# Optimization experiments

Measured on AMD Instinct MI355X. Metric: run time of the kernel, lower is better.

Reference implementation:

```python
import jax, jax.numpy as jnp
import numpy as np

B, S, D_IN, D_OUT, N_EXPERTS = 8, 4096, 512, 512, 8


def setup_inputs() -> dict:
    key = jax.random.key(0)
    k1, k2, k3, k4 = jax.random.split(key, 4)
    x = jax.random.normal(k1, (B, S, D_IN), dtype=jnp.float32)
    partitions = jax.random.randint(k2, (B, S), 0, N_EXPERTS, dtype=jnp.int32)
    # per-branch nn.Linear weights: [n, out_features, in_features], kaiming-ish scale
    W = jax.random.normal(k3, (N_EXPERTS, D_OUT, D_IN), dtype=jnp.float32) * 0.03
    b = jax.random.normal(k4, (N_EXPERTS, D_OUT), dtype=jnp.float32) * 0.01
    return {"x": x, "partitions": partitions, "W": W, "b": b}


def reference(x, partitions, W, b):
    # Hard token partition -> per-branch linear -> scatter combine.
    # Equivalent math to dynamic_partition + branch Linear + dynamic_stitch:
    # out[t] = x[t] @ W[p[t]].T + b[p[t]]
    in_shape = x.shape
    xf = x.reshape(-1, in_shape[-1])          # [T, d_in]
    p = partitions.reshape(-1)                # [T]
    # Compute all-expert outputs, then select per-token expert (vectorized
    # replacement for the variable-size per-partition GEMM loop).
    y = jnp.einsum('td,eod->teo', xf, W) + b[None, :, :]   # [T, n, d_out]
    out = jnp.take_along_axis(y, p[:, None, None], axis=1)[:, 0, :]  # [T, d_out]
    return out.reshape(in_shape[:-1] + (W.shape[1],))
```

## Files before the change

### kernel.cpp

```cpp
#include <hip/hip_runtime.h>
#include <hip/hip_bf16.h>

#define N_EXPERTS 8
#define T_TOKENS 32768
#define D 512
#define TILE 128
#define BK 64
#define NT 4
#define LT_MAX 256
#define GEMM_GRID (N_EXPERTS * LT_MAX * NT)
#define SCATTER_BLOCKS (T_TOKENS / 256)
#define CONVW_BLOCKS ((N_EXPERTS * D * D) / (8 * 256))

typedef __bf16 bf16x8 __attribute__((ext_vector_type(8)));
typedef float  f32x4  __attribute__((ext_vector_type(4)));
typedef unsigned short u16x8 __attribute__((ext_vector_type(8)));

__device__ __forceinline__ unsigned short f2bf(float f) {
    unsigned int u = __float_as_uint(f);
    u += 0x7FFFu + ((u >> 16) & 1u);
    return (unsigned short)(u >> 16);
}

__device__ __forceinline__ u16x8 cvt8(float4 a, float4 b) {
    u16x8 o;
    o[0] = f2bf(a.x); o[1] = f2bf(a.y); o[2] = f2bf(a.z); o[3] = f2bf(a.w);
    o[4] = f2bf(b.x); o[5] = f2bf(b.y); o[6] = f2bf(b.z); o[7] = f2bf(b.w);
    return o;
}

__device__ __forceinline__ void gl2lds16(const void* g, void* l) {
    __builtin_amdgcn_global_load_lds(
        (const __attribute__((address_space(1))) void*)g,
        (__attribute__((address_space(3))) void*)l, 16, 0, 0);
}

__global__ __launch_bounds__(256) void prep_kernel(
        const int* __restrict__ p, int* __restrict__ fill, int* __restrict__ sorted,
        const float* __restrict__ W, unsigned short* __restrict__ Wb) {
    int bid = blockIdx.x;
    int tid = threadIdx.x;
    if (bid < SCATTER_BLOCKS) {
        __shared__ int lcount[N_EXPERTS];
        __shared__ int lbase[N_EXPERTS];
        if (tid < N_EXPERTS) lcount[tid] = 0;
        __syncthreads();
        int t = bid * 256 + tid;
        int e = p[t];
        int lrank = atomicAdd(&lcount[e], 1);
        __syncthreads();
        if (tid < N_EXPERTS)
            lbase[tid] = (lcount[tid] > 0) ? atomicAdd(&fill[tid], lcount[tid]) : 0;
        __syncthreads();
        sorted[e * T_TOKENS + (lbase[e] + 1 + lrank)] = t;
    } else {
        size_t i = ((size_t)(bid - SCATTER_BLOCKS) * 256 + tid) * 8;
        float4 a = *(const float4*)(W + i);
        float4 b = *(const float4*)(W + i + 4);
        *(u16x8*)&Wb[i] = cvt8(a, b);
    }
}

__global__ __launch_bounds__(256, 3) void moe_gemm_fused(
        const float* __restrict__ x, const unsigned short* __restrict__ Wb,
        const float* __restrict__ bias, const int* __restrict__ fill,
        const int* __restrict__ sorted, float* __restrict__ out) {
    __shared__ int s_idx[TILE];
    __shared__ unsigned short sA[TILE * BK];
    __shared__ unsigned short sB[2][TILE * BK];

    int bid = blockIdx.x;
    int e = bid & 7;
    int cnt = fill[e] + 1;
    int j = bid >> 3;
    int lt = j >> 2, bn = j & 3;
    int row0 = lt * TILE;
    if (row0 >= cnt) return;

    int tid = threadIdx.x;
    if (tid < TILE) {
        int r = row0 + tid;
        s_idx[tid] = (r < cnt) ? sorted[e * T_TOKENS + r] : -1;
    }
    __syncthreads();

    int wave = tid >> 6, lane = tid & 63;
    int wm = (wave >> 1) * 64, wn = (wave & 1) * 64;
    int lrow = lane & 15, lq = lane >> 4;
    int srow = lane >> 3, scol = lane & 7, swz = scol ^ srow;

    const float* aptr[4];
#pragma unroll
    for (int t = 0; t < 4; t++) {
        int tok = s_idx[wave * 32 + t * 8 + srow];
        aptr[t] = x + (size_t)(tok < 0 ? 0 : tok) * D + swz * 8;
    }
    const unsigned short* gB = Wb + (size_t)e * D * D
                             + (size_t)(bn * TILE + wave * 32 + srow) * D + swz * 8;

#pragma unroll
    for (int t = 0; t < 4; t++)
        gl2lds16(gB + (size_t)(t * 8) * D, &sB[0][(wave * 32 + t * 8) * BK]);
    __builtin_amdgcn_sched_barrier(0);
    float4 pa[8];
#pragma unroll
    for (int t = 0; t < 4; t++) {
        pa[2 * t]     = *(const float4*)(aptr[t]);
        pa[2 * t + 1] = *(const float4*)(aptr[t] + 4);
    }

    f32x4 acc[4][4];
#pragma unroll
    for (int i = 0; i < 4; i++)
#pragma unroll
        for (int j2 = 0; j2 < 4; j2++)
            acc[i][j2] = (f32x4){0.f, 0.f, 0.f, 0.f};

#pragma unroll
    for (int step = 0; step < 8; step++) {
        const int kk = step * BK;
        asm volatile("s_waitcnt lgkmcnt(0)" ::: "memory");
        __builtin_amdgcn_s_barrier();
        __builtin_amdgcn_sched_barrier(0);
#pragma unroll
        for (int t = 0; t < 4; t++) {
            u16x8 av = cvt8(pa[2 * t], pa[2 * t + 1]);
            *(u16x8*)&sA[(wave * 32 + t * 8 + srow) * BK + scol * 8] = av;
        }
        __builtin_amdgcn_sched_barrier(0);
        if (step < 7) {
#pragma unroll
            for (int t = 0; t < 4; t++)
                gl2lds16(gB + (size_t)(t * 8) * D + kk + BK,
                         &sB[(step + 1) & 1][(wave * 32 + t * 8) * BK]);
            __builtin_amdgcn_sched_barrier(0);
#pragma unroll
            for (int t = 0; t < 4; t++) {
                pa[2 * t]     = *(const float4*)(aptr[t] + kk + BK);
                pa[2 * t + 1] = *(const float4*)(aptr[t] + kk + BK + 4);
            }
            __builtin_amdgcn_sched_barrier(0);
        }
        asm volatile("s_waitcnt lgkmcnt(0)" ::: "memory");
        __builtin_amdgcn_s_barrier();
        __builtin_amdgcn_sched_barrier(0);
        const unsigned short* sBc = sB[step & 1];
#pragma unroll
        for (int ks = 0; ks < 2; ks++) {
            bf16x8 af[4], bfr[4];
#pragma unroll
            for (int i = 0; i < 4; i++) {
                int row = wm + 16 * i + lrow;
                int cb = (ks * 4 + lq) ^ (lrow & 7);
                af[i] = *(const bf16x8*)&sA[row * BK + cb * 8];
            }
#pragma unroll
            for (int j2 = 0; j2 < 4; j2++) {
                int row = wn + 16 * j2 + lrow;
                int cb = (ks * 4 + lq) ^ (lrow & 7);
                bfr[j2] = *(const bf16x8*)&sBc[row * BK + cb * 8];
            }
#pragma unroll
            for (int i = 0; i < 4; i++)
#pragma unroll
                for (int j2 = 0; j2 < 4; j2++)
                    acc[i][j2] = __builtin_amdgcn_mfma_f32_16x16x32_bf16(
                        af[i], bfr[j2], acc[i][j2], 0, 0, 0);
        }
    }

#pragma unroll
    for (int j2 = 0; j2 < 4; j2++) {
        int ng = bn * TILE + wn + 16 * j2 + lrow;
        float bv = bias[e * D + ng];
#pragma unroll
        for (int i = 0; i < 4; i++) {
#pragma unroll
            for (int r = 0; r < 4; r++) {
                int mrow = wm + 16 * i + lq * 4 + r;
                int tok = s_idx[mrow];
                if (tok >= 0)
                    out[(size_t)tok * D + ng] = acc[i][j2][r] + bv;
            }
        }
    }
}

__global__ __launch_bounds__(256) void moe_gemm_f32(
        const float* __restrict__ x, const float* __restrict__ W,
        const float* __restrict__ bias, const int* __restrict__ fill,
        const int* __restrict__ sorted, float* __restrict__ out) {
    __shared__ int s_idx[TILE];
    __shared__ unsigned short sA[TILE][BK + 8];
    __shared__ unsigned short sB[TILE][BK + 8];

    int bid = blockIdx.x;
    int e = bid & 7;
    int cnt = fill[e] + 1;
    int j = bid >> 3;
    int lt = j >> 2, bn = j & 3;
    int row0 = lt * TILE;
    if (row0 >= cnt) return;

    int tid = threadIdx.x;
    if (tid < TILE) {
        int r = row0 + tid;
        s_idx[tid] = (r < cnt) ? sorted[e * T_TOKENS + r] : -1;
    }
    __syncthreads();

    const float* Wb = W + (size_t)e * D * D + (size_t)(bn * TILE) * D;

    f32x4 acc[4][4];
#pragma unroll
    for (int i = 0; i < 4; i++)
#pragma unroll
        for (int j2 = 0; j2 < 4; j2++)
            acc[i][j2] = (f32x4){0.f, 0.f, 0.f, 0.f};

    int wave = tid >> 6, lane = tid & 63;
    int wm = (wave >> 1) * 64, wn = (wave & 1) * 64;
    int lrow = lane & 15, lq = lane >> 4;

    for (int kk = 0; kk < D; kk += BK) {
#pragma unroll
        for (int i = 0; i < 8; i++) {
            int flat = tid + i * 256;
            int r = flat >> 4, c = (flat & 15) << 2;
            int tok = s_idx[r];
            float4 v = make_float4(0.f, 0.f, 0.f, 0.f);
            if (tok >= 0) v = *(const float4*)(x + (size_t)tok * D + kk + c);
            ushort4 w4;
            w4.x = f2bf(v.x); w4.y = f2bf(v.y); w4.z = f2bf(v.z); w4.w = f2bf(v.w);
            *(ushort4*)&sA[r][c] = w4;
        }
#pragma unroll
        for (int i = 0; i < 8; i++) {
            int flat = tid + i * 256;
            int r = flat >> 4, c = (flat & 15) << 2;
            float4 v = *(const float4*)(Wb + (size_t)r * D + kk + c);
            ushort4 w4;
            w4.x = f2bf(v.x); w4.y = f2bf(v.y); w4.z = f2bf(v.z); w4.w = f2bf(v.w);
            *(ushort4*)&sB[r][c] = w4;
        }
        __syncthreads();
#pragma unroll
        for (int ks = 0; ks < 2; ks++) {
            bf16x8 af[4], bfr[4];
#pragma unroll
            for (int i = 0; i < 4; i++)
                af[i] = *(const bf16x8*)&sA[wm + 16 * i + lrow][ks * 32 + lq * 8];
#pragma unroll
            for (int j2 = 0; j2 < 4; j2++)
                bfr[j2] = *(const bf16x8*)&sB[wn + 16 * j2 + lrow][ks * 32 + lq * 8];
#pragma unroll
            for (int i = 0; i < 4; i++)
#pragma unroll
                for (int j2 = 0; j2 < 4; j2++)
                    acc[i][j2] = __builtin_amdgcn_mfma_f32_16x16x32_bf16(
                        af[i], bfr[j2], acc[i][j2], 0, 0, 0);
        }
        __syncthreads();
    }

#pragma unroll
    for (int j2 = 0; j2 < 4; j2++) {
        int ng = bn * TILE + wn + 16 * j2 + lrow;
        float bv = bias[e * D + ng];
#pragma unroll
        for (int i = 0; i < 4; i++) {
#pragma unroll
            for (int r = 0; r < 4; r++) {
                int mrow = wm + 16 * i + lq * 4 + r;
                int tok = s_idx[mrow];
                if (tok >= 0)
                    out[(size_t)tok * D + ng] = acc[i][j2][r] + bv;
            }
        }
    }
}

extern "C" void kernel_launch(void* const* d_in, const int* in_sizes, int n_in,
                              void* d_out, int out_size, void* d_ws, size_t ws_size,
                              hipStream_t stream) {
    const float* x    = (const float*)d_in[0];
    const int*   part = (const int*)d_in[1];
    const float* W    = (const float*)d_in[2];
    const float* b    = (const float*)d_in[3];
    float* out = (float*)d_out;

    const size_t wb_elems     = (size_t)N_EXPERTS * D * D;
    const size_t sorted_elems = (size_t)N_EXPERTS * T_TOKENS;
    const size_t fast_bytes   = wb_elems * 2 + (sorted_elems + 8) * 4;
    const size_t slow_bytes   = (sorted_elems + 8) * 4;

    if (ws_size >= fast_bytes) {
        unsigned short* Wb = (unsigned short*)d_ws;
        int* sorted = (int*)(Wb + wb_elems);
        int* fill   = sorted + sorted_elems;

        hipMemsetAsync(fill, 0xFF, N_EXPERTS * sizeof(int), stream);
        prep_kernel<<<SCATTER_BLOCKS + CONVW_BLOCKS, 256, 0, stream>>>(
            part, fill, sorted, W, Wb);
        moe_gemm_fused<<<GEMM_GRID, 256, 0, stream>>>(x, Wb, b, fill, sorted, out);
    } else if (ws_size >= slow_bytes) {
        int* sorted = (int*)d_ws;
        int* fill   = sorted + sorted_elems;

        hipMemsetAsync(fill, 0xFF, N_EXPERTS * sizeof(int), stream);
        prep_kernel<<<SCATTER_BLOCKS, 256, 0, stream>>>(
            part, fill, sorted, W, (unsigned short*)nullptr);
        moe_gemm_f32<<<GEMM_GRID, 256, 0, stream>>>(x, W, b, fill, sorted, out);
    }
}
```

Measured before the change: 167.9 us.

## Pre-convert activations to bf16 and stream both GEMM operands via direct-to-LDS loads

The prep kernel now also converts x to a bf16 workspace copy. The GEMM kernel then loads both the gathered token rows and the weights with global_load_lds into a double-buffered LDS tile, removing per-step register conversion and the LDS writes for A. It also adds a wave priority bump around the MFMA block and lowers launch bounds to 2 waves per SIMD. The epilogue stages results through LDS so output rows are written as coalesced 16-byte stores. The cost is an extra full pass over x (read f32, write bf16), more workspace, and more LDS per block.

```diff
diff --git a/kernel.cpp b/kernel.cpp
--- a/kernel.cpp
+++ b/kernel.cpp
@@ -11,6 +11,7 @@
 #define GEMM_GRID (N_EXPERTS * LT_MAX * NT)
 #define SCATTER_BLOCKS (T_TOKENS / 256)
 #define CONVW_BLOCKS ((N_EXPERTS * D * D) / (8 * 256))
+#define CONVX_BLOCKS ((T_TOKENS * D) / (8 * 256))
 
 typedef __bf16 bf16x8 __attribute__((ext_vector_type(8)));
 typedef float  f32x4  __attribute__((ext_vector_type(4)));
@@ -37,7 +38,8 @@
 
 __global__ __launch_bounds__(256) void prep_kernel(
         const int* __restrict__ p, int* __restrict__ fill, int* __restrict__ sorted,
-        const float* __restrict__ W, unsigned short* __restrict__ Wb) {
+        const float* __restrict__ W, unsigned short* __restrict__ Wb,
+        const float* __restrict__ x, unsigned short* __restrict__ xb) {
     int bid = blockIdx.x;
     int tid = threadIdx.x;
     if (bid < SCATTER_BLOCKS) {
@@ -53,21 +55,25 @@
             lbase[tid] = (lcount[tid] > 0) ? atomicAdd(&fill[tid], lcount[tid]) : 0;
         __syncthreads();
         sorted[e * T_TOKENS + (lbase[e] + 1 + lrank)] = t;
-    } else {
+    } else if (bid < SCATTER_BLOCKS + CONVW_BLOCKS) {
         size_t i = ((size_t)(bid - SCATTER_BLOCKS) * 256 + tid) * 8;
         float4 a = *(const float4*)(W + i);
         float4 b = *(const float4*)(W + i + 4);
         *(u16x8*)&Wb[i] = cvt8(a, b);
-    }
-}
-
-__global__ __launch_bounds__(256, 3) void moe_gemm_fused(
-        const float* __restrict__ x, const unsigned short* __restrict__ Wb,
+    } else {
+        size_t i = ((size_t)(bid - SCATTER_BLOCKS - CONVW_BLOCKS) * 256 + tid) * 8;
+        float4 a = *(const float4*)(x + i);
+        float4 b = *(const float4*)(x + i + 4);
+        *(u16x8*)&xb[i] = cvt8(a, b);
+    }
+}
+
+__global__ __launch_bounds__(256, 2) void moe_gemm_dma(
+        const unsigned short* __restrict__ xb, const unsigned short* __restrict__ Wb,
         const float* __restrict__ bias, const int* __restrict__ fill,
         const int* __restrict__ sorted, float* __restrict__ out) {
     __shared__ int s_idx[TILE];
-    __shared__ unsigned short sA[TILE * BK];
-    __shared__ unsigned short sB[2][TILE * BK];
+    __shared__ unsigned short buf[2][2][TILE * BK];
 
     int bid = blockIdx.x;
     int e = bid & 7;
@@ -89,25 +95,22 @@
     int lrow = lane & 15, lq = lane >> 4;
     int srow = lane >> 3, scol = lane & 7, swz = scol ^ srow;
 
-    const float* aptr[4];
+    const unsigned short* gA[4];
 #pragma unroll
     for (int t = 0; t < 4; t++) {
         int tok = s_idx[wave * 32 + t * 8 + srow];
-        aptr[t] = x + (size_t)(tok < 0 ? 0 : tok) * D + swz * 8;
+        gA[t] = xb + (size_t)(tok < 0 ? 0 : tok) * D + swz * 8;
     }
     const unsigned short* gB = Wb + (size_t)e * D * D
                              + (size_t)(bn * TILE + wave * 32 + srow) * D + swz * 8;
 
-#pragma unroll
-    for (int t = 0; t < 4; t++)
-        gl2lds16(gB + (size_t)(t * 8) * D, &sB[0][(wave * 32 + t * 8) * BK]);
-    __builtin_amdgcn_sched_barrier(0);
-    float4 pa[8];
-#pragma unroll
-    for (int t = 0; t < 4; t++) {
-        pa[2 * t]     = *(const float4*)(aptr[t]);
-        pa[2 * t + 1] = *(const float4*)(aptr[t] + 4);
-    }
+#define STAGE(K, KB) do {                                                     \
+    _Pragma("unroll") for (int t = 0; t < 4; t++)                             \
+        gl2lds16(gA[t] + (K) * BK, &buf[KB][0][(wave * 32 + t * 8) * BK]);    \
+    _Pragma("unroll") for (int t = 0; t < 4; t++)                             \
+        gl2lds16(gB + (size_t)(t * 8) * D + (K) * BK,                         \
+                 &buf[KB][1][(wave * 32 + t * 8) * BK]);                      \
+} while (0)
 
     f32x4 acc[4][4];
 #pragma unroll
@@ -116,35 +119,25 @@
         for (int j2 = 0; j2 < 4; j2++)
             acc[i][j2] = (f32x4){0.f, 0.f, 0.f, 0.f};
 
+    STAGE(0, 0);
+
 #pragma unroll
     for (int step = 0; step < 8; step++) {
-        const int kk = step * BK;
         asm volatile("s_waitcnt lgkmcnt(0)" ::: "memory");
         __builtin_amdgcn_s_barrier();
         __builtin_amdgcn_sched_barrier(0);
-#pragma unroll
-        for (int t = 0; t < 4; t++) {
-            u16x8 av = cvt8(pa[2 * t], pa[2 * t + 1]);
-            *(u16x8*)&sA[(wave * 32 + t * 8 + srow) * BK + scol * 8] = av;
-        }
-        __builtin_amdgcn_sched_barrier(0);
         if (step < 7) {
-#pragma unroll
-            for (int t = 0; t < 4; t++)
-                gl2lds16(gB + (size_t)(t * 8) * D + kk + BK,
-                         &sB[(step + 1) & 1][(wave * 32 + t * 8) * BK]);
+            STAGE(step + 1, (step + 1) & 1);
             __builtin_amdgcn_sched_barrier(0);
-#pragma unroll
-            for (int t = 0; t < 4; t++) {
-                pa[2 * t]     = *(const float4*)(aptr[t] + kk + BK);
-                pa[2 * t + 1] = *(const float4*)(aptr[t] + kk + BK + 4);
-            }
-            __builtin_amdgcn_sched_barrier(0);
-        }
-        asm volatile("s_waitcnt lgkmcnt(0)" ::: "memory");
+            asm volatile("s_waitcnt vmcnt(8)" ::: "memory");
+        } else {
+            asm volatile("s_waitcnt vmcnt(0)" ::: "memory");
+        }
         __builtin_amdgcn_s_barrier();
         __builtin_amdgcn_sched_barrier(0);
-        const unsigned short* sBc = sB[step & 1];
+        const unsigned short* sA = buf[step & 1][0];
+        const unsigned short* sB = buf[step & 1][1];
+        __builtin_amdgcn_s_setprio(1);
 #pragma unroll
         for (int ks = 0; ks < 2; ks++) {
             bf16x8 af[4], bfr[4];
@@ -158,7 +151,7 @@
             for (int j2 = 0; j2 < 4; j2++) {
                 int row = wn + 16 * j2 + lrow;
                 int cb = (ks * 4 + lq) ^ (lrow & 7);
-                bfr[j2] = *(const bf16x8*)&sBc[row * BK + cb * 8];
+                bfr[j2] = *(const bf16x8*)&sB[row * BK + cb * 8];
             }
 #pragma unroll
             for (int i = 0; i < 4; i++)
@@ -167,21 +160,45 @@
                     acc[i][j2] = __builtin_amdgcn_mfma_f32_16x16x32_bf16(
                         af[i], bfr[j2], acc[i][j2], 0, 0, 0);
         }
-    }
+        __builtin_amdgcn_s_setprio(0);
+    }
+#undef STAGE
 
 #pragma unroll
     for (int j2 = 0; j2 < 4; j2++) {
-        int ng = bn * TILE + wn + 16 * j2 + lrow;
-        float bv = bias[e * D + ng];
-#pragma unroll
-        for (int i = 0; i < 4; i++) {
-#pragma unroll
-            for (int r = 0; r < 4; r++) {
-                int mrow = wm + 16 * i + lq * 4 + r;
-                int tok = s_idx[mrow];
-                if (tok >= 0)
-                    out[(size_t)tok * D + ng] = acc[i][j2][r] + bv;
-            }
+        float bv = bias[e * D + bn * TILE + wn + 16 * j2 + lrow];
+#pragma unroll
+        for (int i = 0; i < 4; i++)
+#pragma unroll
+            for (int r = 0; r < 4; r++)
+                acc[i][j2][r] += bv;
+    }
+
+    float* ct = (float*)&buf[0][0][0];
+#pragma unroll
+    for (int p = 0; p < 2; p++) {
+        asm volatile("s_waitcnt lgkmcnt(0)" ::: "memory");
+        __builtin_amdgcn_s_barrier();
+        if ((wave >> 1) == p) {
+#pragma unroll
+            for (int j2 = 0; j2 < 4; j2++)
+#pragma unroll
+                for (int i = 0; i < 4; i++)
+#pragma unroll
+                    for (int r = 0; r < 4; r++)
+                        ct[(16 * i + lq * 4 + r) * TILE + wn + 16 * j2 + lrow]
+                            = acc[i][j2][r];
+        }
+        asm volatile("s_waitcnt lgkmcnt(0)" ::: "memory");
+        __builtin_amdgcn_s_barrier();
+#pragma unroll
+        for (int k = 0; k < 8; k++) {
+            int u = tid + 256 * k;
+            int row = u >> 5, ch = u & 31;
+            int tok = s_idx[p * 64 + row];
+            f32x4 v = *(const f32x4*)&ct[row * TILE + ch * 4];
+            if (tok >= 0)
+                *(f32x4*)&out[(size_t)tok * D + bn * TILE + ch * 4] = v;
         }
     }
 }
@@ -209,7 +226,7 @@
     }
     __syncthreads();
 
-    const float* Wb = W + (size_t)e * D * D + (size_t)(bn * TILE) * D;
+    const float* Wbp = W + (size_t)e * D * D + (size_t)(bn * TILE) * D;
 
     f32x4 acc[4][4];
 #pragma unroll
@@ -238,7 +255,7 @@
         for (int i = 0; i < 8; i++) {
             int flat = tid + i * 256;
             int r = flat >> 4, c = (flat & 15) << 2;
-            float4 v = *(const float4*)(Wb + (size_t)r * D + kk + c);
+            float4 v = *(const float4*)(Wbp + (size_t)r * D + kk + c);
             ushort4 w4;
             w4.x = f2bf(v.x); w4.y = f2bf(v.y); w4.z = f2bf(v.z); w4.w = f2bf(v.w);
             *(ushort4*)&sB[r][c] = w4;
@@ -289,27 +306,30 @@
     const float* b    = (const float*)d_in[3];
     float* out = (float*)d_out;
 
+    const size_t xb_elems     = (size_t)T_TOKENS * D;
     const size_t wb_elems     = (size_t)N_EXPERTS * D * D;
     const size_t sorted_elems = (size_t)N_EXPERTS * T_TOKENS;
-    const size_t fast_bytes   = wb_elems * 2 + (sorted_elems + 8) * 4;
+    const size_t fast_bytes   = (xb_elems + wb_elems) * 2 + (sorted_elems + 8) * 4;
     const size_t slow_bytes   = (sorted_elems + 8) * 4;
 
     if (ws_size >= fast_bytes) {
-        unsigned short* Wb = (unsigned short*)d_ws;
+        unsigned short* xb = (unsigned short*)d_ws;
+        unsigned short* Wb = xb + xb_elems;
         int* sorted = (int*)(Wb + wb_elems);
         int* fill   = sorted + sorted_elems;
 
         hipMemsetAsync(fill, 0xFF, N_EXPERTS * sizeof(int), stream);
-        prep_kernel<<<SCATTER_BLOCKS + CONVW_BLOCKS, 256, 0, stream>>>(
-            part, fill, sorted, W, Wb);
-        moe_gemm_fused<<<GEMM_GRID, 256, 0, stream>>>(x, Wb, b, fill, sorted, out);
+        prep_kernel<<<SCATTER_BLOCKS + CONVW_BLOCKS + CONVX_BLOCKS, 256, 0, stream>>>(
+            part, fill, sorted, W, Wb, x, xb);
+        moe_gemm_dma<<<GEMM_GRID, 256, 0, stream>>>(xb, Wb, b, fill, sorted, out);
     } else if (ws_size >= slow_bytes) {
         int* sorted = (int*)d_ws;
         int* fill   = sorted + sorted_elems;
 
         hipMemsetAsync(fill, 0xFF, N_EXPERTS * sizeof(int), stream);
         prep_kernel<<<SCATTER_BLOCKS, 256, 0, stream>>>(
-            part, fill, sorted, W, (unsigned short*)nullptr);
+            part, fill, sorted, W, (unsigned short*)nullptr,
+            x, (unsigned short*)nullptr);
         moe_gemm_f32<<<GEMM_GRID, 256, 0, stream>>>(x, W, b, fill, sorted, out);
     }
 }
```

Result: faster. 153.6 us (-8.5%).

## Load A fragments directly to registers and compact the GEMM grid

Applied to the files above, without the earlier changes.

Replaces the fused GEMM with a variant where each wave loads its own A rows straight from global memory into MFMA register fragments, converting them to bf16 in registers and dropping the sA shared-memory round trip. The wave tiling changes from 64x64 to 32x128, so every wave reads all of B. The grid is compacted to a fixed count of workgroups that map onto the actual per-expert tiles, instead of launching the maximum grid and exiting early. Output goes through an LDS transpose so stores are coalesced 16-byte rows, and s_setprio is raised around the MFMA block. The cost is uncoalesced per-lane A loads and more LDS reads of B per wave.

```diff
diff --git a/kernel.cpp b/kernel.cpp
--- a/kernel.cpp
+++ b/kernel.cpp
@@ -9,6 +9,7 @@
 #define NT 4
 #define LT_MAX 256
 #define GEMM_GRID (N_EXPERTS * LT_MAX * NT)
+#define GRID_WG 1056
 #define SCATTER_BLOCKS (T_TOKENS / 256)
 #define CONVW_BLOCKS ((N_EXPERTS * D * D) / (8 * 256))
 
@@ -61,13 +62,172 @@
     }
 }
 
-__global__ __launch_bounds__(256, 3) void moe_gemm_fused(
+__global__ __launch_bounds__(256, 3) void moe_gemm_rs(
         const float* __restrict__ x, const unsigned short* __restrict__ Wb,
         const float* __restrict__ bias, const int* __restrict__ fill,
         const int* __restrict__ sorted, float* __restrict__ out) {
     __shared__ int s_idx[TILE];
-    __shared__ unsigned short sA[TILE * BK];
     __shared__ unsigned short sB[2][TILE * BK];
+
+    int bid = blockIdx.x;
+    int w6 = bid >> 3;
+    int m = (bid & 7) + (w6 >> 2) * 8;
+    int bn = w6 & 3;
+
+    int e = 0, lt = 0, tacc = 0, found = 0, cnt_e = 0;
+#pragma unroll
+    for (int i = 0; i < N_EXPERTS; i++) {
+        int c = fill[i] + 1;
+        int tiles = (c + TILE - 1) >> 7;
+        if (!found && m < tacc + tiles) { e = i; lt = m - tacc; cnt_e = c; found = 1; }
+        tacc += tiles;
+    }
+    if (!found) return;
+    int row0 = lt * TILE;
+
+    int tid = threadIdx.x;
+    if (tid < TILE) {
+        int r = row0 + tid;
+        s_idx[tid] = (r < cnt_e) ? sorted[e * T_TOKENS + r] : -1;
+    }
+    __syncthreads();
+
+    int wave = tid >> 6, lane = tid & 63;
+    int lrow = lane & 15, lq = lane >> 4;
+    int srow = lane >> 3, scol = lane & 7, swz = scol ^ srow;
+
+    const float* ax[2];
+#pragma unroll
+    for (int mb = 0; mb < 2; mb++) {
+        int tok = s_idx[wave * 32 + mb * 16 + lrow];
+        ax[mb] = x + (size_t)(tok < 0 ? 0 : tok) * D + lq * 8;
+    }
+    const unsigned short* gB = Wb + (size_t)e * D * D
+                             + (size_t)(bn * TILE + wave * 32 + srow) * D + swz * 8;
+
+#define STAGE_B(K, KB) do {                                                   \
+    _Pragma("unroll") for (int t = 0; t < 4; t++)                             \
+        gl2lds16(gB + (size_t)(t * 8) * D + (K) * BK,                         \
+                 &sB[KB][(wave * 32 + t * 8) * BK]);                          \
+} while (0)
+
+#define LOAD_A(K, SB) do {                                                    \
+    _Pragma("unroll") for (int mb = 0; mb < 2; mb++)                          \
+    _Pragma("unroll") for (int ks = 0; ks < 2; ks++) {                        \
+        raw[SB][mb][ks][0] = *(const float4*)(ax[mb] + (K) * BK + ks * 32);   \
+        raw[SB][mb][ks][1] = *(const float4*)(ax[mb] + (K) * BK + ks * 32 + 4);\
+    }                                                                         \
+} while (0)
+
+    float4 raw[2][2][2][2];
+    f32x4 acc[2][8];
+#pragma unroll
+    for (int mb = 0; mb < 2; mb++)
+#pragma unroll
+        for (int nj = 0; nj < 8; nj++)
+            acc[mb][nj] = (f32x4){0.f, 0.f, 0.f, 0.f};
+
+    STAGE_B(0, 0);
+    __builtin_amdgcn_sched_barrier(0);
+    LOAD_A(0, 0);
+    __builtin_amdgcn_sched_barrier(0);
+
+#pragma unroll
+    for (int step = 0; step < 8; step++) {
+        asm volatile("s_waitcnt lgkmcnt(0)" ::: "memory");
+        __builtin_amdgcn_s_barrier();
+        __builtin_amdgcn_sched_barrier(0);
+        if (step < 7) {
+            STAGE_B(step + 1, (step + 1) & 1);
+            __builtin_amdgcn_sched_barrier(0);
+            asm volatile("s_waitcnt vmcnt(4)" ::: "memory");
+        } else {
+            asm volatile("s_waitcnt vmcnt(0)" ::: "memory");
+        }
+        __builtin_amdgcn_sched_barrier(0);
+        bf16x8 af[2][2];
+#pragma unroll
+        for (int mb = 0; mb < 2; mb++)
+#pragma unroll
+            for (int ks = 0; ks < 2; ks++) {
+                u16x8 t = cvt8(raw[step & 1][mb][ks][0], raw[step & 1][mb][ks][1]);
+                af[mb][ks] = *(bf16x8*)&t;
+            }
+        if (step < 7) {
+            LOAD_A(step + 1, (step + 1) & 1);
+            __builtin_amdgcn_sched_barrier(0);
+        }
+        __builtin_amdgcn_s_barrier();
+        __builtin_amdgcn_sched_barrier(0);
+        const unsigned short* sBc = sB[step & 1];
+        __builtin_amdgcn_s_setprio(1);
+#pragma unroll
+        for (int ks = 0; ks < 2; ks++) {
+            bf16x8 bfr[8];
+#pragma unroll
+            for (int nj = 0; nj < 8; nj++) {
+                int row = 16 * nj + lrow;
+                int cb = (ks * 4 + lq) ^ (lrow & 7);
+                bfr[nj] = *(const bf16x8*)&sBc[row * BK + cb * 8];
+            }
+#pragma unroll
+            for (int mb = 0; mb < 2; mb++)
+#pragma unroll
+                for (int nj = 0; nj < 8; nj++)
+                    acc[mb][nj] = __builtin_amdgcn_mfma_f32_16x16x32_bf16(
+                        af[mb][ks], bfr[nj], acc[mb][nj], 0, 0, 0);
+        }
+        __builtin_amdgcn_s_setprio(0);
+    }
+#undef STAGE_B
+#undef LOAD_A
+
+#pragma unroll
+    for (int nj = 0; nj < 8; nj++) {
+        float bv = bias[e * D + bn * TILE + 16 * nj + lrow];
+#pragma unroll
+        for (int mb = 0; mb < 2; mb++)
+#pragma unroll
+            for (int r = 0; r < 4; r++)
+                acc[mb][nj][r] += bv;
+    }
+
+    float* ct = (float*)&sB[0][0];
+#pragma unroll
+    for (int p = 0; p < 2; p++) {
+        asm volatile("s_waitcnt lgkmcnt(0)" ::: "memory");
+        __builtin_amdgcn_s_barrier();
+        if ((wave >> 1) == p) {
+#pragma unroll
+            for (int mb = 0; mb < 2; mb++)
+#pragma unroll
+                for (int nj = 0; nj < 8; nj++)
+#pragma unroll
+                    for (int r = 0; r < 4; r++)
+                        ct[((wave & 1) * 32 + 16 * mb + lq * 4 + r) * TILE
+                           + 16 * nj + lrow] = acc[mb][nj][r];
+        }
+        asm volatile("s_waitcnt lgkmcnt(0)" ::: "memory");
+        __builtin_amdgcn_s_barrier();
+#pragma unroll
+        for (int k = 0; k < 8; k++) {
+            int u = tid + 256 * k;
+            int row = u >> 5, ch = u & 31;
+            int tok = s_idx[p * 64 + row];
+            f32x4 v = *(const f32x4*)&ct[row * TILE + ch * 4];
+            if (tok >= 0)
+                *(f32x4*)&out[(size_t)tok * D + bn * TILE + ch * 4] = v;
+        }
+    }
+}
+
+__global__ __launch_bounds__(256) void moe_gemm_f32(
+        const float* __restrict__ x, const float* __restrict__ W,
+        const float* __restrict__ bias, const int* __restrict__ fill,
+        const int* __restrict__ sorted, float* __restrict__ out) {
+    __shared__ int s_idx[TILE];
+    __shared__ unsigned short sA[TILE][BK + 8];
+    __shared__ unsigned short sB[TILE][BK + 8];
 
     int bid = blockIdx.x;
     int e = bid & 7;
@@ -84,132 +244,7 @@
     }
     __syncthreads();
 
-    int wave = tid >> 6, lane = tid & 63;
-    int wm = (wave >> 1) * 64, wn = (wave & 1) * 64;
-    int lrow = lane & 15, lq = lane >> 4;
-    int srow = lane >> 3, scol = lane & 7, swz = scol ^ srow;
-
-    const float* aptr[4];
-#pragma unroll
-    for (int t = 0; t < 4; t++) {
-        int tok = s_idx[wave * 32 + t * 8 + srow];
-        aptr[t] = x + (size_t)(tok < 0 ? 0 : tok) * D + swz * 8;
-    }
-    const unsigned short* gB = Wb + (size_t)e * D * D
-                             + (size_t)(bn * TILE + wave * 32 + srow) * D + swz * 8;
-
-#pragma unroll
-    for (int t = 0; t < 4; t++)
-        gl2lds16(gB + (size_t)(t * 8) * D, &sB[0][(wave * 32 + t * 8) * BK]);
-    __builtin_amdgcn_sched_barrier(0);
-    float4 pa[8];
-#pragma unroll
-    for (int t = 0; t < 4; t++) {
-        pa[2 * t]     = *(const float4*)(aptr[t]);
-        pa[2 * t + 1] = *(const float4*)(aptr[t] + 4);
-    }
-
-    f32x4 acc[4][4];
-#pragma unroll
-    for (int i = 0; i < 4; i++)
-#pragma unroll
-        for (int j2 = 0; j2 < 4; j2++)
-            acc[i][j2] = (f32x4){0.f, 0.f, 0.f, 0.f};
-
-#pragma unroll
-    for (int step = 0; step < 8; step++) {
-        const int kk = step * BK;
-        asm volatile("s_waitcnt lgkmcnt(0)" ::: "memory");
-        __builtin_amdgcn_s_barrier();
-        __builtin_amdgcn_sched_barrier(0);
-#pragma unroll
-        for (int t = 0; t < 4; t++) {
-            u16x8 av = cvt8(pa[2 * t], pa[2 * t + 1]);
-            *(u16x8*)&sA[(wave * 32 + t * 8 + srow) * BK + scol * 8] = av;
-        }
-        __builtin_amdgcn_sched_barrier(0);
-        if (step < 7) {
-#pragma unroll
-            for (int t = 0; t < 4; t++)
-                gl2lds16(gB + (size_t)(t * 8) * D + kk + BK,
-                         &sB[(step + 1) & 1][(wave * 32 + t * 8) * BK]);
-            __builtin_amdgcn_sched_barrier(0);
-#pragma unroll
-            for (int t = 0; t < 4; t++) {
-                pa[2 * t]     = *(const float4*)(aptr[t] + kk + BK);
-                pa[2 * t + 1] = *(const float4*)(aptr[t] + kk + BK + 4);
-            }
-            __builtin_amdgcn_sched_barrier(0);
-        }
-        asm volatile("s_waitcnt lgkmcnt(0)" ::: "memory");
-        __builtin_amdgcn_s_barrier();
-        __builtin_amdgcn_sched_barrier(0);
-        const unsigned short* sBc = sB[step & 1];
-#pragma unroll
-        for (int ks = 0; ks < 2; ks++) {
-            bf16x8 af[4], bfr[4];
-#pragma unroll
-            for (int i = 0; i < 4; i++) {
-                int row = wm + 16 * i + lrow;
-                int cb = (ks * 4 + lq) ^ (lrow & 7);
-                af[i] = *(const bf16x8*)&sA[row * BK + cb * 8];
-            }
-#pragma unroll
-            for (int j2 = 0; j2 < 4; j2++) {
-                int row = wn + 16 * j2 + lrow;
-                int cb = (ks * 4 + lq) ^ (lrow & 7);
-                bfr[j2] = *(const bf16x8*)&sBc[row * BK + cb * 8];
-            }
-#pragma unroll
-            for (int i = 0; i < 4; i++)
-#pragma unroll
-                for (int j2 = 0; j2 < 4; j2++)
-                    acc[i][j2] = __builtin_amdgcn_mfma_f32_16x16x32_bf16(
-                        af[i], bfr[j2], acc[i][j2], 0, 0, 0);
-        }
-    }
-
-#pragma unroll
-    for (int j2 = 0; j2 < 4; j2++) {
-        int ng = bn * TILE + wn + 16 * j2 + lrow;
-        float bv = bias[e * D + ng];
-#pragma unroll
-        for (int i = 0; i < 4; i++) {
-#pragma unroll
-            for (int r = 0; r < 4; r++) {
-                int mrow = wm + 16 * i + lq * 4 + r;
-                int tok = s_idx[mrow];
-                if (tok >= 0)
-                    out[(size_t)tok * D + ng] = acc[i][j2][r] + bv;
-            }
-        }
-    }
-}
-
-__global__ __launch_bounds__(256) void moe_gemm_f32(
-        const float* __restrict__ x, const float* __restrict__ W,
-        const float* __restrict__ bias, const int* __restrict__ fill,
-        const int* __restrict__ sorted, float* __restrict__ out) {
-    __shared__ int s_idx[TILE];
-    __shared__ unsigned short sA[TILE][BK + 8];
-    __shared__ unsigned short sB[TILE][BK + 8];
-
-    int bid = blockIdx.x;
-    int e = bid & 7;
-    int cnt = fill[e] + 1;
-    int j = bid >> 3;
-    int lt = j >> 2, bn = j & 3;
-    int row0 = lt * TILE;
-    if (row0 >= cnt) return;
-
-    int tid = threadIdx.x;
-    if (tid < TILE) {
-        int r = row0 + tid;
-        s_idx[tid] = (r < cnt) ? sorted[e * T_TOKENS + r] : -1;
-    }
-    __syncthreads();
-
-    const float* Wb = W + (size_t)e * D * D + (size_t)(bn * TILE) * D;
+    const float* Wbp = W + (size_t)e * D * D + (size_t)(bn * TILE) * D;
 
     f32x4 acc[4][4];
 #pragma unroll
@@ -238,7 +273,7 @@
         for (int i = 0; i < 8; i++) {
             int flat = tid + i * 256;
             int r = flat >> 4, c = (flat & 15) << 2;
-            float4 v = *(const float4*)(Wb + (size_t)r * D + kk + c);
+            float4 v = *(const float4*)(Wbp + (size_t)r * D + kk + c);
             ushort4 w4;
             w4.x = f2bf(v.x); w4.y = f2bf(v.y); w4.z = f2bf(v.z); w4.w = f2bf(v.w);
             *(ushort4*)&sB[r][c] = w4;
@@ -302,7 +337,7 @@
         hipMemsetAsync(fill, 0xFF, N_EXPERTS * sizeof(int), stream);
         prep_kernel<<<SCATTER_BLOCKS + CONVW_BLOCKS, 256, 0, stream>>>(
             part, fill, sorted, W, Wb);
-        moe_gemm_fused<<<GEMM_GRID, 256, 0, stream>>>(x, Wb, b, fill, sorted, out);
+        moe_gemm_rs<<<GRID_WG, 256, 0, stream>>>(x, Wb, b, fill, sorted, out);
     } else if (ws_size >= slow_bytes) {
         int* sorted = (int*)d_ws;
         int* fill   = sorted + sorted_elems;
```

New measurement: 176.0 us. 4.8% more time.
